# Optimization experiments

Hardware: AMD Instinct MI355X
Metric: run time of the kernel (lower is better)

The kernel has to match this reference:

```python
import jax, jax.numpy as jnp
import numpy as np

DIM = 256
HEADS = 8
HEAD_DIM = DIM // HEADS
HIDDEN = DIM * 4


def layer_norm(x, w, b, eps=1e-5):
    m = jnp.mean(x, axis=-1, keepdims=True)
    v = jnp.mean((x - m) ** 2, axis=-1, keepdims=True)
    return (x - m) / jnp.sqrt(v + eps) * w + b


def setup_inputs() -> dict:
    key = jax.random.key(0)
    ks = jax.random.split(key, 12)
    s = lambda fan_in: 1.0 / np.sqrt(fan_in)
    inp = {
        "x0": jax.random.normal(ks[0], (2, 32, 64, DIM), jnp.float32),
        "x1": jax.random.normal(ks[1], (2, 32, 64, DIM), jnp.float32),
        # torch Linear weights stored [out, in], no bias for qk/v/merge
        "qk_w": jax.random.uniform(ks[2], (DIM, DIM), jnp.float32, -s(DIM), s(DIM)),
        "v_w": jax.random.uniform(ks[3], (DIM, DIM), jnp.float32, -s(DIM), s(DIM)),
        "merge_w": jax.random.uniform(ks[4], (DIM, DIM), jnp.float32, -s(DIM), s(DIM)),
        "ln1_w": jnp.ones((DIM,), jnp.float32),
        "ln1_b": jnp.zeros((DIM,), jnp.float32),
        "ln2_w": jnp.ones((DIM,), jnp.float32),
        "ln2_b": jnp.zeros((DIM,), jnp.float32),
        "fc1_w": jax.random.uniform(ks[5], (HIDDEN, 2 * DIM), jnp.float32, -s(2 * DIM), s(2 * DIM)),
        "fc1_b": jnp.zeros((HIDDEN,), jnp.float32),
        "fc2_w": jax.random.uniform(ks[6], (DIM, HIDDEN), jnp.float32, -s(HIDDEN), s(HIDDEN)),
        "fc2_b": jnp.zeros((DIM,), jnp.float32),
        "gamma": jnp.ones((DIM,), jnp.float32),
    }
    return inp


def reference(x0, x1, qk_w, v_w, merge_w, ln1_w, ln1_b, ln2_w, ln2_b,
              fc1_w, fc1_b, fc2_w, fc2_b, gamma):
    N0, L0, WW0, C = x0.shape
    N1, L1, WW1, _ = x1.shape
    x0f = x0.reshape(N0, L0 * WW0, C)
    x1f = x1.reshape(N1, L1 * WW1, C)

    n0 = layer_norm(x0f, ln1_w, ln1_b)
    n1 = layer_norm(x1f, ln1_w, ln1_b)

    def heads(t):  # [N, S, C] -> [N, H, S, Dh]
        N, S, _ = t.shape
        return t.reshape(N, S, HEADS, HEAD_DIM).transpose(0, 2, 1, 3)

    scale = HEAD_DIM ** -0.25  # sqrt of softmax_temp, applied to both sides
    qk0 = heads(n0 @ qk_w.T) * scale
    qk1 = heads(n1 @ qk_w.T) * scale
    v0 = heads(n0 @ v_w.T)
    v1 = heads(n1 @ v_w.T)

    # shared score matrix, reused for both softmax directions
    sim = jnp.einsum('bhld,bhsd->bhls', qk0, qk1)  # [N,H,L,S]
    attn01 = jax.nn.softmax(sim, axis=-1)
    attn10 = jax.nn.softmax(sim, axis=-2)  # == softmax(sim^T, -1)^T

    m0 = jnp.einsum('bhls,bhsd->bhld', attn01, v1)
    m1 = jnp.einsum('bhls,bhld->bhsd', attn10, v0)

    def unheads(t):  # [N,H,S,Dh] -> [N,S,C]
        N, H, S, D = t.shape
        return t.transpose(0, 2, 1, 3).reshape(N, S, H * D)

    m0 = unheads(m0) @ merge_w.T
    m1 = unheads(m1) @ merge_w.T

    def ffn_residual(x, m):
        h = jnp.concatenate([x, m], axis=-1)
        h = jax.nn.gelu(h @ fc1_w.T + fc1_b, approximate=False)
        h = h @ fc2_w.T + fc2_b
        return x + gamma * layer_norm(h, ln2_w, ln2_b)

    y0 = ffn_residual(x0f, m0).reshape(N0, L0, WW0, C)
    y1 = ffn_residual(x1f, m1).reshape(N1, L1, WW1, C)
    return (y0, y1)
```

## Files before the change

kernel.cpp:

```cpp
#include <hip/hip_runtime.h>
#include <hip/hip_bf16.h>
#include <math.h>


typedef float  f32x4  __attribute__((ext_vector_type(4)));
typedef __bf16 bf16x8 __attribute__((ext_vector_type(8)));

#define MFMA16(A, B, C) __builtin_amdgcn_mfma_f32_16x16x32_bf16((A), (B), (C), 0, 0, 0)

static constexpr int   ROWS  = 8192;
static constexpr float QK_SCALE = 0.42044820762685725f * 1.2011224087864498f;

__device__ inline unsigned short f2b(float f) {
    __hip_bfloat16 h = __float2bfloat16(f);
    union { __hip_bfloat16 h; unsigned short u; } cv;
    cv.h = h;
    return cv.u;
}

__device__ inline float exp2_fast(float x) {
#if __has_builtin(__builtin_amdgcn_exp2f)
    return __builtin_amdgcn_exp2f(x);
#else
    return __exp2f(x);
#endif
}

__device__ inline float gelu_f(float x) {
    float z = 0.7978845608028654f * (x + 0.044715f * x * x * x);
    z = fminf(fmaxf(z, -15.0f), 15.0f);
    const float e = __expf(-2.0f * z);
    const float t = (1.0f - e) / (1.0f + e);
    return 0.5f * x * (1.0f + t);
}

__global__ __launch_bounds__(256) void prep_kernel(
    const float* __restrict__ qkw, const float* __restrict__ vw,
    const float* __restrict__ mw,  const float* __restrict__ w1,
    const float* __restrict__ w2,  unsigned short* __restrict__ o,
    const float* __restrict__ x0,  const float* __restrict__ x1,
    const float* __restrict__ lw,  const float* __restrict__ lb,
    unsigned short* __restrict__ nb, unsigned short* __restrict__ acat)
{
    if (blockIdx.x < 3840) {
        int i = blockIdx.x * 256 + threadIdx.x;
        float v;
        if      (i <  65536) v = qkw[i];
        else if (i < 131072) v = vw[i - 65536];
        else if (i < 196608) v = mw[i - 131072];
        else if (i < 720896) v = w1[i - 196608];
        else                 v = w2[i - 720896];
        o[i] = f2b(v);
        return;
    }
    const int wid  = threadIdx.x >> 6;
    const int lane = threadIdx.x & 63;
    const int row  = (blockIdx.x - 3840) * 4 + wid;
    const float* xr = (row < 4096) ? (x0 + (size_t)row * 256)
                                   : (x1 + (size_t)(row - 4096) * 256);
    const int c0 = lane * 4;
    const float4 xv = *(const float4*)(xr + c0);
    float s  = (xv.x + xv.y) + (xv.z + xv.w);
    float sq = (xv.x * xv.x + xv.y * xv.y) + (xv.z * xv.z + xv.w * xv.w);
#pragma unroll
    for (int off = 1; off < 64; off <<= 1) {
        s  += __shfl_xor(s,  off);
        sq += __shfl_xor(sq, off);
    }
    const float mean = s * (1.0f / 256.0f);
    const float var  = sq * (1.0f / 256.0f) - mean * mean;
    const float rs   = rsqrtf(var + 1e-5f);
    const float4 wv4 = *(const float4*)(lw + c0);
    const float4 bv4 = *(const float4*)(lb + c0);
    ushort4 nv;
    nv.x = f2b((xv.x - mean) * rs * wv4.x + bv4.x);
    nv.y = f2b((xv.y - mean) * rs * wv4.y + bv4.y);
    nv.z = f2b((xv.z - mean) * rs * wv4.z + bv4.z);
    nv.w = f2b((xv.w - mean) * rs * wv4.w + bv4.w);
    *(ushort4*)(nb + (size_t)row * 256 + c0) = nv;
    ushort4 xb;
    xb.x = f2b(xv.x); xb.y = f2b(xv.y); xb.z = f2b(xv.z); xb.w = f2b(xv.w);
    *(ushort4*)(acat + (size_t)row * 512 + c0) = xb;
}

__global__ __launch_bounds__(256) void gemm_qkv(
    const unsigned short* __restrict__ A, const unsigned short* __restrict__ W,
    unsigned short* __restrict__ qkb, unsigned short* __restrict__ vtb)
{
    constexpr int K = 256;
    __shared__ unsigned short As[64 * 72];
    __shared__ unsigned short Ws[64 * 72];
    const int tid  = threadIdx.x;
    const int wid  = tid >> 6;
    const int lane = tid & 63;
    const int ln   = lane & 15;
    const int quad = lane >> 4;
    const int m0 = blockIdx.x * 64, n0 = blockIdx.y * 64;
    f32x4 acc[4] = {{0,0,0,0},{0,0,0,0},{0,0,0,0},{0,0,0,0}};
    const int srow = tid >> 3;
    const int skc  = (tid & 7) * 8;
    const unsigned short* aP0 = A + (size_t)(m0 + srow)      * K + skc;
    const unsigned short* aP1 = A + (size_t)(m0 + srow + 32) * K + skc;
    const unsigned short* wP0 = W + (size_t)(n0 + srow)      * K + skc;
    const unsigned short* wP1 = W + (size_t)(n0 + srow + 32) * K + skc;
    for (int k0 = 0; k0 < K; k0 += 64) {
        *(uint4*)(As + srow * 72 + skc)        = *(const uint4*)(aP0 + k0);
        *(uint4*)(As + (srow + 32) * 72 + skc) = *(const uint4*)(aP1 + k0);
        *(uint4*)(Ws + srow * 72 + skc)        = *(const uint4*)(wP0 + k0);
        *(uint4*)(Ws + (srow + 32) * 72 + skc) = *(const uint4*)(wP1 + k0);
        __syncthreads();
#pragma unroll
        for (int kk = 0; kk < 64; kk += 32) {
            const bf16x8 af = *(const bf16x8*)(As + (wid * 16 + ln) * 72 + kk + quad * 8);
#pragma unroll
            for (int f = 0; f < 4; ++f) {
                const bf16x8 wf = *(const bf16x8*)(Ws + (f * 16 + ln) * 72 + kk + quad * 8);
                acc[f] = MFMA16(wf, af, acc[f]);
            }
        }
        __syncthreads();
    }
    const int rowm = m0 + wid * 16 + ln;
    if (n0 < 256) {
#pragma unroll
        for (int f = 0; f < 4; ++f) {
            const int cb = n0 + f * 16 + quad * 4;
            ushort4 o;
            o.x = f2b(acc[f][0] * QK_SCALE); o.y = f2b(acc[f][1] * QK_SCALE);
            o.z = f2b(acc[f][2] * QK_SCALE); o.w = f2b(acc[f][3] * QK_SCALE);
            *(ushort4*)(qkb + (size_t)rowm * 256 + cb) = o;
        }
    } else {
#pragma unroll
        for (int f = 0; f < 4; ++f) {
            const int cb = (n0 - 256) + f * 16 + quad * 4;
#pragma unroll
            for (int r = 0; r < 4; ++r)
                vtb[(size_t)(cb + r) * 8192 + rowm] = f2b(acc[f][r]);
        }
    }
}

__global__ __launch_bounds__(256) void gemm_merge(
    const unsigned short* __restrict__ A, const unsigned short* __restrict__ W,
    unsigned short* __restrict__ outB)
{
    constexpr int K = 256;
    __shared__ unsigned short As[64 * 72];
    __shared__ unsigned short Ws[64 * 72];
    const int tid  = threadIdx.x;
    const int wid  = tid >> 6;
    const int lane = tid & 63;
    const int ln   = lane & 15;
    const int quad = lane >> 4;
    const int m0 = blockIdx.x * 64, n0 = blockIdx.y * 64;
    f32x4 acc[4] = {{0,0,0,0},{0,0,0,0},{0,0,0,0},{0,0,0,0}};
    const int srow = tid >> 3;
    const int skc  = (tid & 7) * 8;
    const unsigned short* aP0 = A + (size_t)(m0 + srow)      * K + skc;
    const unsigned short* aP1 = A + (size_t)(m0 + srow + 32) * K + skc;
    const unsigned short* wP0 = W + (size_t)(n0 + srow)      * K + skc;
    const unsigned short* wP1 = W + (size_t)(n0 + srow + 32) * K + skc;
    for (int k0 = 0; k0 < K; k0 += 64) {
        *(uint4*)(As + srow * 72 + skc)        = *(const uint4*)(aP0 + k0);
        *(uint4*)(As + (srow + 32) * 72 + skc) = *(const uint4*)(aP1 + k0);
        *(uint4*)(Ws + srow * 72 + skc)        = *(const uint4*)(wP0 + k0);
        *(uint4*)(Ws + (srow + 32) * 72 + skc) = *(const uint4*)(wP1 + k0);
        __syncthreads();
#pragma unroll
        for (int kk = 0; kk < 64; kk += 32) {
            const bf16x8 af = *(const bf16x8*)(As + (wid * 16 + ln) * 72 + kk + quad * 8);
#pragma unroll
            for (int f = 0; f < 4; ++f) {
                const bf16x8 wf = *(const bf16x8*)(Ws + (f * 16 + ln) * 72 + kk + quad * 8);
                acc[f] = MFMA16(wf, af, acc[f]);
            }
        }
        __syncthreads();
    }
    const int rowm = m0 + wid * 16 + ln;
#pragma unroll
    for (int f = 0; f < 4; ++f) {
        const int cb = n0 + f * 16 + quad * 4;
        ushort4 o;
        o.x = f2b(acc[f][0]); o.y = f2b(acc[f][1]);
        o.z = f2b(acc[f][2]); o.w = f2b(acc[f][3]);
        *(ushort4*)(outB + (size_t)rowm * 512 + 256 + cb) = o;
    }
}

template <bool GELU_, bool OUTB>
__global__ __launch_bounds__(256) void gemm128(
    const unsigned short* __restrict__ A, const unsigned short* __restrict__ W,
    const float* __restrict__ bias,
    unsigned short* __restrict__ outB, float* __restrict__ outF,
    int K, int NS)
{
    __shared__ unsigned short As[128 * 72];
    __shared__ unsigned short Ws[128 * 72];
    const int tid  = threadIdx.x;
    const int wid  = tid >> 6;
    const int lane = tid & 63;
    const int ln   = lane & 15;
    const int quad = lane >> 4;
    const int m0 = blockIdx.x * 128, n0 = blockIdx.y * 128;
    const int wm = (wid & 1) * 64, wn = (wid >> 1) * 64;
    f32x4 acc[4][4];
#pragma unroll
    for (int f = 0; f < 4; ++f)
#pragma unroll
        for (int i = 0; i < 4; ++i) acc[f][i] = (f32x4){0, 0, 0, 0};
    const int sr = tid >> 2;
    const int sc = (tid & 3) * 8;
    for (int k0 = 0; k0 < K; k0 += 64) {
        const unsigned short* aB = A + (size_t)m0 * K + k0;
        const unsigned short* wB = W + (size_t)n0 * K + k0;
        *(uint4*)(As + sr * 72 + sc)             = *(const uint4*)(aB + (size_t)sr * K + sc);
        *(uint4*)(As + sr * 72 + sc + 32)        = *(const uint4*)(aB + (size_t)sr * K + sc + 32);
        *(uint4*)(As + (sr + 64) * 72 + sc)      = *(const uint4*)(aB + (size_t)(sr + 64) * K + sc);
        *(uint4*)(As + (sr + 64) * 72 + sc + 32) = *(const uint4*)(aB + (size_t)(sr + 64) * K + sc + 32);
        *(uint4*)(Ws + sr * 72 + sc)             = *(const uint4*)(wB + (size_t)sr * K + sc);
        *(uint4*)(Ws + sr * 72 + sc + 32)        = *(const uint4*)(wB + (size_t)sr * K + sc + 32);
        *(uint4*)(Ws + (sr + 64) * 72 + sc)      = *(const uint4*)(wB + (size_t)(sr + 64) * K + sc);
        *(uint4*)(Ws + (sr + 64) * 72 + sc + 32) = *(const uint4*)(wB + (size_t)(sr + 64) * K + sc + 32);
        __syncthreads();
#pragma unroll
        for (int kk = 0; kk < 64; kk += 32) {
            bf16x8 af[4], wf[4];
#pragma unroll
            for (int i = 0; i < 4; ++i)
                af[i] = *(const bf16x8*)(As + (wm + i * 16 + ln) * 72 + kk + quad * 8);
#pragma unroll
            for (int f = 0; f < 4; ++f)
                wf[f] = *(const bf16x8*)(Ws + (wn + f * 16 + ln) * 72 + kk + quad * 8);
#pragma unroll
            for (int f = 0; f < 4; ++f)
#pragma unroll
                for (int i = 0; i < 4; ++i)
                    acc[f][i] = MFMA16(wf[f], af[i], acc[f][i]);
        }
        __syncthreads();
    }
#pragma unroll
    for (int f = 0; f < 4; ++f) {
        const int feat = n0 + wn + f * 16 + quad * 4;
        const float4 b4 = *(const float4*)(bias + feat);
#pragma unroll
        for (int i = 0; i < 4; ++i) {
            const int token = m0 + wm + i * 16 + ln;
            float vv[4] = {acc[f][i][0] + b4.x, acc[f][i][1] + b4.y,
                           acc[f][i][2] + b4.z, acc[f][i][3] + b4.w};
            if (GELU_) {
#pragma unroll
                for (int r = 0; r < 4; ++r) vv[r] = gelu_f(vv[r]);
            }
            if (OUTB) {
                ushort4 o;
                o.x = f2b(vv[0]); o.y = f2b(vv[1]); o.z = f2b(vv[2]); o.w = f2b(vv[3]);
                *(ushort4*)(outB + (size_t)token * NS + feat) = o;
            } else {
                float4 o = {vv[0], vv[1], vv[2], vv[3]};
                *(float4*)(outF + (size_t)token * NS + feat) = o;
            }
        }
    }
}

__global__ __launch_bounds__(256, 4) void attn_kernel(
    const unsigned short* __restrict__ qk, const unsigned short* __restrict__ vtb,
    unsigned short* __restrict__ mo)
{
    __shared__ unsigned short Pw[4][64 * 32];
    const int tid  = threadIdx.x;
    const int wid  = tid >> 6;
    const int lane = tid & 63;
    const int ln   = lane & 15;
    const int quad = lane >> 4;
    const int dir = blockIdx.z, bh = blockIdx.y;
    const int b = bh >> 3, h = bh & 7;
    const int qbase = b * 2048 + (dir ? 4096 : 0);
    const int kbase = b * 2048 + (dir ? 0 : 4096);
    const int q0 = blockIdx.x * 64;
    const int xsw = ((ln >> 1) & 1) << 4;

    bf16x8 qf[4];
#pragma unroll
    for (int qg = 0; qg < 4; ++qg)
        qf[qg] = *(const bf16x8*)(qk + (size_t)(qbase + q0 + qg * 16 + ln) * 256 + h * 32 + quad * 8);

    f32x4 oacc[4][2];
#pragma unroll
    for (int qg = 0; qg < 4; ++qg) {
        oacc[qg][0] = (f32x4){0, 0, 0, 0};
        oacc[qg][1] = (f32x4){0, 0, 0, 0};
    }
    float lp[4] = {0.0f, 0.0f, 0.0f, 0.0f};
    const f32x4 zf = {0, 0, 0, 0};

    const unsigned short* kp = qk  + (size_t)(kbase + wid * 32 + ln) * 256 + h * 32 + quad * 8;
    const unsigned short* vp = vtb + (size_t)(h * 32 + ln) * 8192 + (kbase + wid * 32) + quad * 8;

    unsigned short* Pq[4];
#pragma unroll
    for (int qg = 0; qg < 4; ++qg) Pq[qg] = &Pw[wid][(qg * 16 + ln) * 32];

    bf16x8 kc0 = *(const bf16x8*)(kp);
    bf16x8 kc1 = *(const bf16x8*)(kp + 16 * 256);
    bf16x8 vc0 = *(const bf16x8*)(vp);
    bf16x8 vc1 = *(const bf16x8*)(vp + 16 * 8192);
    bf16x8 kn0, kn1, vn0, vn1;

    for (int it = 0; it < 16; ++it) {
#pragma unroll
        for (int sub = 0; sub < 2; ++sub) {
            const bf16x8 kf = sub ? kc1 : kc0;
            f32x4 s[4];
#pragma unroll
            for (int qg = 0; qg < 4; ++qg) s[qg] = MFMA16(kf, qf[qg], zf);
#pragma unroll
            for (int qg = 0; qg < 4; ++qg) {
                const float e0 = exp2_fast(s[qg][0]), e1 = exp2_fast(s[qg][1]);
                const float e2 = exp2_fast(s[qg][2]), e3 = exp2_fast(s[qg][3]);
                lp[qg] += (e0 + e1) + (e2 + e3);
                ushort4 pb;
                pb.x = f2b(e0); pb.y = f2b(e1); pb.z = f2b(e2); pb.w = f2b(e3);
                *(ushort4*)(Pq[qg] + ((sub * 16 + quad * 4) ^ xsw)) = pb;
            }
        }
        if (it < 15) {
            const unsigned short* kpn = kp + (size_t)(it + 1) * 128 * 256;
            const unsigned short* vpn = vp + (it + 1) * 128;
            kn0 = *(const bf16x8*)(kpn);
            kn1 = *(const bf16x8*)(kpn + 16 * 256);
            vn0 = *(const bf16x8*)(vpn);
            vn1 = *(const bf16x8*)(vpn + 16 * 8192);
        }
        asm volatile("s_waitcnt lgkmcnt(0)" ::: "memory");
#pragma unroll
        for (int qg = 0; qg < 4; ++qg) {
            const bf16x8 pf = *(const bf16x8*)(Pq[qg] + ((quad * 8) ^ xsw));
            oacc[qg][0] = MFMA16(vc0, pf, oacc[qg][0]);
            oacc[qg][1] = MFMA16(vc1, pf, oacc[qg][1]);
        }
        if (it < 15) { kc0 = kn0; kc1 = kn1; vc0 = vn0; vc1 = vn1; }
    }

#pragma unroll
    for (int qg = 0; qg < 4; ++qg) {
        lp[qg] += __shfl_xor(lp[qg], 16);
        lp[qg] += __shfl_xor(lp[qg], 32);
    }
    __syncthreads();
    float* scr  = (float*)&Pw[0][0];
    float* Lbuf = scr;
    float* Obuf = scr + 256;
    if (quad == 0) {
#pragma unroll
        for (int qg = 0; qg < 4; ++qg) Lbuf[wid * 64 + qg * 16 + ln] = lp[qg];
    }
#pragma unroll
    for (int qg = 0; qg < 4; ++qg) {
#pragma unroll
        for (int dg = 0; dg < 2; ++dg)
            *(f32x4*)&Obuf[(wid * 2 + dg) * 256 + lane * 4] = oacc[qg][dg];
        __syncthreads();
        if (wid == qg) {
            const int q = qg * 16 + ln;
            const float rinv = 1.0f /
                (Lbuf[q] + Lbuf[64 + q] + Lbuf[128 + q] + Lbuf[192 + q]);
            const size_t orow = (size_t)(qbase + q0 + q) * 256 + h * 32;
#pragma unroll
            for (int dg = 0; dg < 2; ++dg) {
                f32x4 sum = *(f32x4*)&Obuf[(0 + dg) * 256 + lane * 4];
#pragma unroll
                for (int w = 1; w < 4; ++w)
                    sum += *(f32x4*)&Obuf[(w * 2 + dg) * 256 + lane * 4];
                ushort4 o;
                o.x = f2b(sum[0] * rinv); o.y = f2b(sum[1] * rinv);
                o.z = f2b(sum[2] * rinv); o.w = f2b(sum[3] * rinv);
                *(ushort4*)(mo + orow + dg * 16 + quad * 4) = o;
            }
        }
        __syncthreads();
    }
}

__global__ __launch_bounds__(256) void ln_out_kernel(
    const float* __restrict__ x0, const float* __restrict__ x1,
    const float* __restrict__ h2, const float* __restrict__ w,
    const float* __restrict__ b,  const float* __restrict__ gamma,
    float* __restrict__ out)
{
    const int wid  = threadIdx.x >> 6;
    const int lane = threadIdx.x & 63;
    const int row  = blockIdx.x * 4 + wid;
    const int c0 = lane * 4;
    const float4 hv = *(const float4*)(h2 + (size_t)row * 256 + c0);
    float s  = (hv.x + hv.y) + (hv.z + hv.w);
    float sq = (hv.x * hv.x + hv.y * hv.y) + (hv.z * hv.z + hv.w * hv.w);
#pragma unroll
    for (int off = 1; off < 64; off <<= 1) {
        s  += __shfl_xor(s,  off);
        sq += __shfl_xor(sq, off);
    }
    const float mean = s * (1.0f / 256.0f);
    const float var  = sq * (1.0f / 256.0f) - mean * mean;
    const float rs   = rsqrtf(var + 1e-5f);
    const float* xr = (row < 4096) ? (x0 + (size_t)row * 256)
                                   : (x1 + (size_t)(row - 4096) * 256);
    const float4 xv = *(const float4*)(xr + c0);
    const float4 w4 = *(const float4*)(w + c0);
    const float4 b4 = *(const float4*)(b + c0);
    const float4 g4 = *(const float4*)(gamma + c0);
    float4 y;
    y.x = xv.x + g4.x * ((hv.x - mean) * rs * w4.x + b4.x);
    y.y = xv.y + g4.y * ((hv.y - mean) * rs * w4.y + b4.y);
    y.z = xv.z + g4.z * ((hv.z - mean) * rs * w4.z + b4.z);
    y.w = xv.w + g4.w * ((hv.w - mean) * rs * w4.w + b4.w);
    *(float4*)(out + (size_t)row * 256 + c0) = y;
}

extern "C" void kernel_launch(void* const* d_in, const int* in_sizes, int n_in,
                              void* d_out, int out_size, void* d_ws, size_t ws_size,
                              hipStream_t stream) {
    (void)in_sizes; (void)n_in; (void)out_size; (void)ws_size;
    const float* x0      = (const float*)d_in[0];
    const float* x1      = (const float*)d_in[1];
    const float* qk_w    = (const float*)d_in[2];
    const float* v_w     = (const float*)d_in[3];
    const float* merge_w = (const float*)d_in[4];
    const float* ln1_w   = (const float*)d_in[5];
    const float* ln1_b   = (const float*)d_in[6];
    const float* ln2_w   = (const float*)d_in[7];
    const float* ln2_b   = (const float*)d_in[8];
    const float* fc1_w   = (const float*)d_in[9];
    const float* fc1_b   = (const float*)d_in[10];
    const float* fc2_w   = (const float*)d_in[11];
    const float* fc2_b   = (const float*)d_in[12];
    const float* gamma   = (const float*)d_in[13];
    float* out = (float*)d_out;

    unsigned short* nb   = (unsigned short*)d_ws;
    unsigned short* qkb  = nb   + (size_t)ROWS * 256;
    unsigned short* vtb  = qkb  + (size_t)ROWS * 256;
    unsigned short* mb   = vtb  + (size_t)ROWS * 256;
    unsigned short* acat = mb   + (size_t)ROWS * 256;
    unsigned short* fc1o = acat + (size_t)ROWS * 512;
    float*          h2   = (float*)(fc1o + (size_t)ROWS * 1024);
    unsigned short* wqv  = (unsigned short*)(h2 + (size_t)ROWS * 256);
    unsigned short* wm   = wqv + 131072;
    unsigned short* w1   = wm  + 65536;
    unsigned short* w2   = w1  + 524288;

    prep_kernel<<<5888, 256, 0, stream>>>(
        qk_w, v_w, merge_w, fc1_w, fc2_w, wqv,
        x0, x1, ln1_w, ln1_b, nb, acat);

    gemm_qkv<<<dim3(128, 8), 256, 0, stream>>>(nb, wqv, qkb, vtb);

    attn_kernel<<<dim3(32, 16, 2), 256, 0, stream>>>(qkb, vtb, mb);

    gemm_merge<<<dim3(128, 4), 256, 0, stream>>>(mb, wm, acat);

    gemm128<true, true><<<dim3(64, 8), 256, 0, stream>>>(
        acat, w1, fc1_b, fc1o, nullptr, 512, 1024);
    gemm128<false, false><<<dim3(64, 2), 256, 0, stream>>>(
        fc1o, w2, fc2_b, nullptr, h2, 1024, 256);

    ln_out_kernel<<<2048, 256, 0, stream>>>(x0, x1, h2, ln2_w, ln2_b, gamma, out);
}
```

Before: 183.2 us.

## Fold merge projection into fc1 weights and drop the merge GEMM

The merge linear layer is folded algebraically into the second half of fc1, precomputing fc1_w[:,256:] @ merge_w inside the prep kernel with a small MFMA tile GEMM. The attention kernel then writes its output straight into the second half of the concatenated fc1 input, so the separate gemm_merge launch and its intermediate buffer go away. In exchange, a 1024x256x256 weight GEMM runs on every call, and the fused weight is rounded to bf16 after the product, which slightly changes numerics.

```diff
diff --git a/kernel.cpp b/kernel.cpp
--- a/kernel.cpp
+++ b/kernel.cpp
@@ -42,45 +42,104 @@
     const float* __restrict__ lw,  const float* __restrict__ lb,
     unsigned short* __restrict__ nb, unsigned short* __restrict__ acat)
 {
-    if (blockIdx.x < 3840) {
+    __shared__ unsigned short As[64 * 72];
+    __shared__ unsigned short Ws[64 * 72];
+    if (blockIdx.x < 2560) {
         int i = blockIdx.x * 256 + threadIdx.x;
-        float v;
-        if      (i <  65536) v = qkw[i];
-        else if (i < 131072) v = vw[i - 65536];
-        else if (i < 196608) v = mw[i - 131072];
-        else if (i < 720896) v = w1[i - 196608];
-        else                 v = w2[i - 720896];
-        o[i] = f2b(v);
+        if      (i <  65536) o[i] = f2b(qkw[i]);
+        else if (i < 131072) o[i] = f2b(vw[i - 65536]);
+        else if (i < 393216) {
+            int j = i - 131072, r = j >> 8, c = j & 255;
+            o[131072 + r * 512 + c] = f2b(w1[(size_t)r * 512 + c]);
+        } else {
+            o[i + 262144] = f2b(w2[i - 393216]);
+        }
         return;
     }
-    const int wid  = threadIdx.x >> 6;
-    const int lane = threadIdx.x & 63;
-    const int row  = (blockIdx.x - 3840) * 4 + wid;
-    const float* xr = (row < 4096) ? (x0 + (size_t)row * 256)
-                                   : (x1 + (size_t)(row - 4096) * 256);
-    const int c0 = lane * 4;
-    const float4 xv = *(const float4*)(xr + c0);
-    float s  = (xv.x + xv.y) + (xv.z + xv.w);
-    float sq = (xv.x * xv.x + xv.y * xv.y) + (xv.z * xv.z + xv.w * xv.w);
-#pragma unroll
-    for (int off = 1; off < 64; off <<= 1) {
-        s  += __shfl_xor(s,  off);
-        sq += __shfl_xor(sq, off);
-    }
-    const float mean = s * (1.0f / 256.0f);
-    const float var  = sq * (1.0f / 256.0f) - mean * mean;
-    const float rs   = rsqrtf(var + 1e-5f);
-    const float4 wv4 = *(const float4*)(lw + c0);
-    const float4 bv4 = *(const float4*)(lb + c0);
-    ushort4 nv;
-    nv.x = f2b((xv.x - mean) * rs * wv4.x + bv4.x);
-    nv.y = f2b((xv.y - mean) * rs * wv4.y + bv4.y);
-    nv.z = f2b((xv.z - mean) * rs * wv4.z + bv4.z);
-    nv.w = f2b((xv.w - mean) * rs * wv4.w + bv4.w);
-    *(ushort4*)(nb + (size_t)row * 256 + c0) = nv;
-    ushort4 xb;
-    xb.x = f2b(xv.x); xb.y = f2b(xv.y); xb.z = f2b(xv.z); xb.w = f2b(xv.w);
-    *(ushort4*)(acat + (size_t)row * 512 + c0) = xb;
+    if (blockIdx.x < 4608) {
+        const int wid  = threadIdx.x >> 6;
+        const int lane = threadIdx.x & 63;
+        const int row  = (blockIdx.x - 2560) * 4 + wid;
+        const float* xr = (row < 4096) ? (x0 + (size_t)row * 256)
+                                       : (x1 + (size_t)(row - 4096) * 256);
+        const int c0 = lane * 4;
+        const float4 xv = *(const float4*)(xr + c0);
+        float s  = (xv.x + xv.y) + (xv.z + xv.w);
+        float sq = (xv.x * xv.x + xv.y * xv.y) + (xv.z * xv.z + xv.w * xv.w);
+#pragma unroll
+        for (int off = 1; off < 64; off <<= 1) {
+            s  += __shfl_xor(s,  off);
+            sq += __shfl_xor(sq, off);
+        }
+        const float mean = s * (1.0f / 256.0f);
+        const float var  = sq * (1.0f / 256.0f) - mean * mean;
+        const float rs   = rsqrtf(var + 1e-5f);
+        const float4 wv4 = *(const float4*)(lw + c0);
+        const float4 bv4 = *(const float4*)(lb + c0);
+        ushort4 nv;
+        nv.x = f2b((xv.x - mean) * rs * wv4.x + bv4.x);
+        nv.y = f2b((xv.y - mean) * rs * wv4.y + bv4.y);
+        nv.z = f2b((xv.z - mean) * rs * wv4.z + bv4.z);
+        nv.w = f2b((xv.w - mean) * rs * wv4.w + bv4.w);
+        *(ushort4*)(nb + (size_t)row * 256 + c0) = nv;
+        ushort4 xb;
+        xb.x = f2b(xv.x); xb.y = f2b(xv.y); xb.z = f2b(xv.z); xb.w = f2b(xv.w);
+        *(ushort4*)(acat + (size_t)row * 512 + c0) = xb;
+        return;
+    }
+    const int t   = blockIdx.x - 4608;
+    const int i0  = (t >> 2) * 64;
+    const int j0  = (t & 3) * 64;
+    const int tid  = threadIdx.x;
+    const int wid  = tid >> 6;
+    const int lane = tid & 63;
+    const int ln   = lane & 15;
+    const int quad = lane >> 4;
+    f32x4 acc[4] = {{0,0,0,0},{0,0,0,0},{0,0,0,0},{0,0,0,0}};
+    const int srow = tid >> 3;
+    const int skc  = (tid & 7) * 8;
+    for (int k0 = 0; k0 < 256; k0 += 64) {
+#pragma unroll
+        for (int rr = 0; rr < 2; ++rr) {
+            const int row = srow + rr * 32;
+            const float* asrc = w1 + (size_t)(i0 + row) * 512 + 256 + k0 + skc;
+            const float4 f0 = *(const float4*)(asrc);
+            const float4 f1 = *(const float4*)(asrc + 4);
+            ushort4 a0, a1;
+            a0.x = f2b(f0.x); a0.y = f2b(f0.y); a0.z = f2b(f0.z); a0.w = f2b(f0.w);
+            a1.x = f2b(f1.x); a1.y = f2b(f1.y); a1.z = f2b(f1.z); a1.w = f2b(f1.w);
+            *(ushort4*)(As + row * 72 + skc)     = a0;
+            *(ushort4*)(As + row * 72 + skc + 4) = a1;
+            const float* bsrc = mw + (size_t)(k0 + skc) * 256 + (j0 + row);
+            ushort4 b0, b1;
+            b0.x = f2b(bsrc[0 * 256]); b0.y = f2b(bsrc[1 * 256]);
+            b0.z = f2b(bsrc[2 * 256]); b0.w = f2b(bsrc[3 * 256]);
+            b1.x = f2b(bsrc[4 * 256]); b1.y = f2b(bsrc[5 * 256]);
+            b1.z = f2b(bsrc[6 * 256]); b1.w = f2b(bsrc[7 * 256]);
+            *(ushort4*)(Ws + row * 72 + skc)     = b0;
+            *(ushort4*)(Ws + row * 72 + skc + 4) = b1;
+        }
+        __syncthreads();
+#pragma unroll
+        for (int kk = 0; kk < 64; kk += 32) {
+            const bf16x8 af = *(const bf16x8*)(As + (wid * 16 + ln) * 72 + kk + quad * 8);
+#pragma unroll
+            for (int f = 0; f < 4; ++f) {
+                const bf16x8 wf = *(const bf16x8*)(Ws + (f * 16 + ln) * 72 + kk + quad * 8);
+                acc[f] = MFMA16(wf, af, acc[f]);
+            }
+        }
+        __syncthreads();
+    }
+    const int rowm = i0 + wid * 16 + ln;
+#pragma unroll
+    for (int f = 0; f < 4; ++f) {
+        const int cb = j0 + f * 16 + quad * 4;
+        ushort4 ov;
+        ov.x = f2b(acc[f][0]); ov.y = f2b(acc[f][1]);
+        ov.z = f2b(acc[f][2]); ov.w = f2b(acc[f][3]);
+        *(ushort4*)(o + 131072 + (size_t)rowm * 512 + 256 + cb) = ov;
+    }
 }
 
 __global__ __launch_bounds__(256) void gemm_qkv(
@@ -141,54 +200,6 @@
     }
 }
 
-__global__ __launch_bounds__(256) void gemm_merge(
-    const unsigned short* __restrict__ A, const unsigned short* __restrict__ W,
-    unsigned short* __restrict__ outB)
-{
-    constexpr int K = 256;
-    __shared__ unsigned short As[64 * 72];
-    __shared__ unsigned short Ws[64 * 72];
-    const int tid  = threadIdx.x;
-    const int wid  = tid >> 6;
-    const int lane = tid & 63;
-    const int ln   = lane & 15;
-    const int quad = lane >> 4;
-    const int m0 = blockIdx.x * 64, n0 = blockIdx.y * 64;
-    f32x4 acc[4] = {{0,0,0,0},{0,0,0,0},{0,0,0,0},{0,0,0,0}};
-    const int srow = tid >> 3;
-    const int skc  = (tid & 7) * 8;
-    const unsigned short* aP0 = A + (size_t)(m0 + srow)      * K + skc;
-    const unsigned short* aP1 = A + (size_t)(m0 + srow + 32) * K + skc;
-    const unsigned short* wP0 = W + (size_t)(n0 + srow)      * K + skc;
-    const unsigned short* wP1 = W + (size_t)(n0 + srow + 32) * K + skc;
-    for (int k0 = 0; k0 < K; k0 += 64) {
-        *(uint4*)(As + srow * 72 + skc)        = *(const uint4*)(aP0 + k0);
-        *(uint4*)(As + (srow + 32) * 72 + skc) = *(const uint4*)(aP1 + k0);
-        *(uint4*)(Ws + srow * 72 + skc)        = *(const uint4*)(wP0 + k0);
-        *(uint4*)(Ws + (srow + 32) * 72 + skc) = *(const uint4*)(wP1 + k0);
-        __syncthreads();
-#pragma unroll
-        for (int kk = 0; kk < 64; kk += 32) {
-            const bf16x8 af = *(const bf16x8*)(As + (wid * 16 + ln) * 72 + kk + quad * 8);
-#pragma unroll
-            for (int f = 0; f < 4; ++f) {
-                const bf16x8 wf = *(const bf16x8*)(Ws + (f * 16 + ln) * 72 + kk + quad * 8);
-                acc[f] = MFMA16(wf, af, acc[f]);
-            }
-        }
-        __syncthreads();
-    }
-    const int rowm = m0 + wid * 16 + ln;
-#pragma unroll
-    for (int f = 0; f < 4; ++f) {
-        const int cb = n0 + f * 16 + quad * 4;
-        ushort4 o;
-        o.x = f2b(acc[f][0]); o.y = f2b(acc[f][1]);
-        o.z = f2b(acc[f][2]); o.w = f2b(acc[f][3]);
-        *(ushort4*)(outB + (size_t)rowm * 512 + 256 + cb) = o;
-    }
-}
-
 template <bool GELU_, bool OUTB>
 __global__ __launch_bounds__(256) void gemm128(
     const unsigned short* __restrict__ A, const unsigned short* __restrict__ W,
@@ -368,7 +379,7 @@
             const int q = qg * 16 + ln;
             const float rinv = 1.0f /
                 (Lbuf[q] + Lbuf[64 + q] + Lbuf[128 + q] + Lbuf[192 + q]);
-            const size_t orow = (size_t)(qbase + q0 + q) * 256 + h * 32;
+            const size_t orow = (size_t)(qbase + q0 + q) * 512 + 256 + h * 32;
 #pragma unroll
             for (int dg = 0; dg < 2; ++dg) {
                 f32x4 sum = *(f32x4*)&Obuf[(0 + dg) * 256 + lane * 4];
@@ -443,29 +454,25 @@
     unsigned short* nb   = (unsigned short*)d_ws;
     unsigned short* qkb  = nb   + (size_t)ROWS * 256;
     unsigned short* vtb  = qkb  + (size_t)ROWS * 256;
-    unsigned short* mb   = vtb  + (size_t)ROWS * 256;
-    unsigned short* acat = mb   + (size_t)ROWS * 256;
+    unsigned short* acat = vtb  + (size_t)ROWS * 256;
     unsigned short* fc1o = acat + (size_t)ROWS * 512;
     float*          h2   = (float*)(fc1o + (size_t)ROWS * 1024);
     unsigned short* wqv  = (unsigned short*)(h2 + (size_t)ROWS * 256);
-    unsigned short* wm   = wqv + 131072;
-    unsigned short* w1   = wm  + 65536;
-    unsigned short* w2   = w1  + 524288;
-
-    prep_kernel<<<5888, 256, 0, stream>>>(
+    unsigned short* w1f  = wqv + 131072;
+    unsigned short* w2b  = w1f + 524288;
+
+    prep_kernel<<<4672, 256, 0, stream>>>(
         qk_w, v_w, merge_w, fc1_w, fc2_w, wqv,
         x0, x1, ln1_w, ln1_b, nb, acat);
 
     gemm_qkv<<<dim3(128, 8), 256, 0, stream>>>(nb, wqv, qkb, vtb);
 
-    attn_kernel<<<dim3(32, 16, 2), 256, 0, stream>>>(qkb, vtb, mb);
-
-    gemm_merge<<<dim3(128, 4), 256, 0, stream>>>(mb, wm, acat);
+    attn_kernel<<<dim3(32, 16, 2), 256, 0, stream>>>(qkb, vtb, acat);
 
     gemm128<true, true><<<dim3(64, 8), 256, 0, stream>>>(
-        acat, w1, fc1_b, fc1o, nullptr, 512, 1024);
+        acat, w1f, fc1_b, fc1o, nullptr, 512, 1024);
     gemm128<false, false><<<dim3(64, 2), 256, 0, stream>>>(
-        fc1o, w2, fc2_b, nullptr, h2, 1024, 256);
+        fc1o, w2b, fc2_b, nullptr, h2, 1024, 256);
 
     ln_out_kernel<<<2048, 256, 0, stream>>>(x0, x1, h2, ln2_w, ln2_b, gamma, out);
 }
```

Result: no change. 183.7 us (median of 2 runs) (+0.2%).
